# Performance work log

Measured on AMD Instinct MI355X. Metric: run time of the kernel, lower is better.

Reference implementation:

```python
import jax, jax.numpy as jnp
import numpy as np

WS = (8, 8, 8)          # window_size (d, h, w) -- all equal
N_TOK = WS[0] * WS[1] * WS[2]   # 512
DIM = 192
HEADS = 6
HEAD_DIM = DIM // HEADS  # 32
B_ = 64                  # num_windows * batch (batch = 1)


def _build_rel_coords_table():
    # matches torch: meshgrid of arange(-(w-1), w) per axis, normalized, *8, signed log2
    r = np.arange(-(WS[0] - 1), WS[0], dtype=np.float32)
    tab = np.stack(np.meshgrid(r, r, r, indexing='ij'), axis=-1)[None]  # (1,15,15,15,3)
    tab = tab / (WS[0] - 1)
    tab = tab * 8.0
    tab = np.sign(tab) * np.log2(np.abs(tab) + 1.0) / np.log2(8.0)
    return tab.astype(np.float32)


def _build_rel_pos_index():
    c = np.arange(WS[0])
    coords = np.stack(np.meshgrid(c, c, c, indexing='ij'))          # (3, 8, 8, 8)
    flat = coords.reshape(3, -1)                                     # (3, N)
    rel = flat[:, :, None] - flat[:, None, :]                        # (3, N, N)
    rel = rel.transpose(1, 2, 0).copy()                              # (N, N, 3)
    rel += WS[0] - 1
    rel[:, :, 0] *= (2 * WS[1] - 1) * (2 * WS[2] - 1)
    rel[:, :, 1] *= 2 * WS[2] - 1
    return rel.sum(-1).astype(np.int32)                              # (N, N)


def setup_inputs() -> dict:
    key = jax.random.key(0)
    ks = jax.random.split(key, 8)
    x = jax.random.normal(ks[0], (B_, N_TOK, DIM), dtype=jnp.float32)
    # 0 / -inf style additive mask (use large negative finite for stability)
    m = jax.random.uniform(ks[1], (B_, N_TOK, N_TOK))
    mask = jnp.where(m < 0.1, jnp.float32(-1e4), jnp.float32(0.0))
    w_qkv = jax.random.normal(ks[2], (3 * DIM, DIM), dtype=jnp.float32) * (DIM ** -0.5)
    q_bias = jnp.zeros((DIM,), jnp.float32)
    v_bias = jnp.zeros((DIM,), jnp.float32)
    cpb_w1 = jax.random.normal(ks[3], (512, 3), dtype=jnp.float32) * 0.3
    cpb_b1 = jnp.zeros((512,), jnp.float32)
    cpb_w2 = jax.random.normal(ks[4], (HEADS, 512), dtype=jnp.float32) * 0.05
    rel_coords_table = jnp.asarray(_build_rel_coords_table())
    rel_pos_index = jnp.asarray(_build_rel_pos_index())
    return {"x": x, "mask": mask, "w_qkv": w_qkv, "q_bias": q_bias,
            "v_bias": v_bias, "cpb_w1": cpb_w1, "cpb_b1": cpb_b1,
            "cpb_w2": cpb_w2, "rel_coords_table": rel_coords_table,
            "rel_pos_index": rel_pos_index}


def reference(x, mask, w_qkv, q_bias, v_bias, cpb_w1, cpb_b1, cpb_w2,
              rel_coords_table, rel_pos_index):
    Bw, N, C = x.shape
    H, D = HEADS, HEAD_DIM
    # qkv projection with bias = cat(q_bias, zeros, v_bias)
    qkv_bias = jnp.concatenate([q_bias, jnp.zeros_like(v_bias), v_bias])
    qkv = x @ w_qkv.T + qkv_bias                       # (Bw, N, 3C)
    qkv = qkv.reshape(Bw, N, 3, H, D).transpose(2, 0, 3, 1, 4)
    q, k, v = qkv[0], qkv[1], qkv[2]                   # (Bw, H, N, D)
    # continuous position bias MLP: 3 -> 512 -> H
    tab = rel_coords_table.reshape(-1, 3)              # (3375, 3)
    tab = jax.nn.relu(tab @ cpb_w1.T + cpb_b1) @ cpb_w2.T  # (3375, H)
    bias = tab[rel_pos_index.reshape(-1)].reshape(N, N, H)
    bias = 16.0 * jax.nn.sigmoid(bias.transpose(2, 0, 1))  # (H, N, N)
    # SDPA with additive mask (standard 1/sqrt(D) scaling, as in forward_flash)
    scale = jnp.float32(1.0 / np.sqrt(D))
    scores = jnp.einsum('bhnd,bhmd->bhnm', q, k) * scale
    scores = scores + mask[:, None, :, :] + bias[None]
    attn = jax.nn.softmax(scores, axis=-1)
    out = jnp.einsum('bhnm,bhmd->bhnd', attn, v)       # (Bw, H, N, D)
    return out
```

## Files before the change

kernel.cpp:

```cpp
#include <hip/hip_runtime.h>
#include <hip/hip_bf16.h>


typedef __bf16 bf16x8 __attribute__((ext_vector_type(8)));
typedef __bf16 bf16x4v __attribute__((ext_vector_type(4)));
typedef float  f32x4  __attribute__((ext_vector_type(4)));
typedef _Float16 f16x4 __attribute__((ext_vector_type(4)));
typedef _Float16 f16x8 __attribute__((ext_vector_type(8)));
typedef unsigned uint2v __attribute__((ext_vector_type(2)));
typedef int int4v __attribute__((ext_vector_type(4)));
typedef unsigned long long u64;

#define LOG2E 1.4426950408889634f

__device__ __forceinline__ bf16x8 cvt2_bf16x8(f32x4 a, f32x4 b) {
  bf16x8 r;
  r[0] = (__bf16)a[0]; r[1] = (__bf16)a[1]; r[2] = (__bf16)a[2]; r[3] = (__bf16)a[3];
  r[4] = (__bf16)b[0]; r[5] = (__bf16)b[1]; r[6] = (__bf16)b[2]; r[7] = (__bf16)b[3];
  return r;
}

__device__ __forceinline__ unsigned pack2bf(float a, float b) {
  unsigned short ua = __builtin_bit_cast(unsigned short, (__bf16)a);
  unsigned short ub = __builtin_bit_cast(unsigned short, (__bf16)b);
  return (unsigned)ua | ((unsigned)ub << 16);
}

__device__ __forceinline__ bf16x8 frag_from_words(unsigned w0, unsigned w1,
                                                  unsigned w2, unsigned w3) {
  union { unsigned u[4]; bf16x8 v; } f;
  f.u[0] = w0; f.u[1] = w1; f.u[2] = w2; f.u[3] = w3;
  return f.v;
}

#define PREP_MB    2048
#define PREP_WCONV 108
#define PREP_CPB   3375
#define PREP_GRID  (PREP_MB + PREP_WCONV + PREP_CPB)

__global__ __launch_bounds__(256) void prep_kernel(
    const float* __restrict__ w, __bf16* __restrict__ wbf,
    const float* __restrict__ table, const float* __restrict__ w1,
    const float* __restrict__ b1, const float* __restrict__ w2,
    float* __restrict__ tab6,
    const float* __restrict__ m, u64* __restrict__ bits)
{
  __shared__ float red[4][6];
  int blk = blockIdx.x;
  if (blk < PREP_MB) {
    int li8 = threadIdx.x & 7;
    for (size_t t = (size_t)blk * 256 + threadIdx.x;
         t < 2097152ull; t += (size_t)PREP_MB * 256) {
      const float* mp = m + t * 8;
      f32x4 v0 = *(const f32x4*)mp;
      f32x4 v1 = *(const f32x4*)(mp + 4);
      unsigned byte =
          (v0[0] == 0.f ? 1u : 0u)  | (v0[1] == 0.f ? 2u : 0u) |
          (v0[2] == 0.f ? 4u : 0u)  | (v0[3] == 0.f ? 8u : 0u) |
          (v1[0] == 0.f ? 16u : 0u) | (v1[1] == 0.f ? 32u : 0u) |
          (v1[2] == 0.f ? 64u : 0u) | (v1[3] == 0.f ? 128u : 0u);
      u64 part = (u64)byte << (8 * li8);
      part |= __shfl_xor(part, 1);
      part |= __shfl_xor(part, 2);
      part |= __shfl_xor(part, 4);
      if (li8 == 0) {
        int w_ = (int)(t >> 3);
        int b = w_ >> 12, i = (w_ >> 3) & 511, jw = w_ & 7;
        bits[(((size_t)b * 8 + jw) << 9) + i] = part;
      }
    }
  } else if (blk < PREP_MB + PREP_WCONV) {
    int t = (blk - PREP_MB) * 256 + threadIdx.x;
    f32x4 v = *(const f32x4*)(w + (size_t)t * 4);
    bf16x4v o;
    o[0] = (__bf16)v[0]; o[1] = (__bf16)v[1]; o[2] = (__bf16)v[2]; o[3] = (__bf16)v[3];
    *(bf16x4v*)(wbf + (size_t)t * 4) = o;
  } else {
    int p = blk - PREP_MB - PREP_WCONV;
    float c0 = table[p * 3 + 0], c1 = table[p * 3 + 1], c2 = table[p * 3 + 2];
    float acc[6] = {0.f, 0.f, 0.f, 0.f, 0.f, 0.f};
#pragma unroll
    for (int jj = 0; jj < 2; ++jj) {
      int j = threadIdx.x + jj * 256;
      float hv = w1[j * 3 + 0] * c0 + w1[j * 3 + 1] * c1 + w1[j * 3 + 2] * c2 + b1[j];
      hv = fmaxf(hv, 0.0f);
#pragma unroll
      for (int t = 0; t < 6; ++t) acc[t] += w2[t * 512 + j] * hv;
    }
#pragma unroll
    for (int t = 0; t < 6; ++t) {
      acc[t] += __shfl_xor(acc[t], 1);
      acc[t] += __shfl_xor(acc[t], 2);
      acc[t] += __shfl_xor(acc[t], 4);
      acc[t] += __shfl_xor(acc[t], 8);
      acc[t] += __shfl_xor(acc[t], 16);
      acc[t] += __shfl_xor(acc[t], 32);
    }
    int wave = threadIdx.x >> 6;
    if ((threadIdx.x & 63) == 0)
#pragma unroll
      for (int t = 0; t < 6; ++t) red[wave][t] = acc[t];
    __syncthreads();
    if (threadIdx.x < 6) {
      int t = threadIdx.x;
      float s = red[0][t] + red[1][t] + red[2][t] + red[3][t];
      float sig = 16.0f / (1.0f + expf(-s));
      tab6[p * 8 + t] = sig * LOG2E;
    }
  }
}

#define MID_QKV  3072
#define MID_BIAS 342
#define MID_GRID (MID_QKV + MID_BIAS)

__global__ __launch_bounds__(192) void mid_kernel(
    const float* __restrict__ x,
    const __bf16* __restrict__ wbf,
    const float* __restrict__ qb,
    const float* __restrict__ vb,
    __bf16* __restrict__ Qo,
    __bf16* __restrict__ Ko,
    __bf16* __restrict__ Vt,
    const int* __restrict__ relidx,
    const float* __restrict__ tab6,
    _Float16* __restrict__ biasH)
{
  __shared__ __bf16 tile[3][32][72];
  if (blockIdx.x >= MID_QKV) {
    for (int q4 = (blockIdx.x - MID_QKV) * 192 + threadIdx.x; q4 < 65536;
         q4 += MID_BIAS * 192) {
      int ij = q4 * 4;
      int i = ij >> 9, p = ij & 511;
      int jblk = p >> 6, g = (p >> 4) & 3, kf = (p >> 2) & 3;
      int j = (jblk << 6) + kf * 16 + g * 4;
      int4v idx4 = *(const int4v*)(relidx + (i << 9) + j);
      float val[6][4];
#pragma unroll
      for (int u = 0; u < 4; ++u) {
        f32x4 lo = *(const f32x4*)(tab6 + (size_t)idx4[u] * 8);
        f32x4 hi = *(const f32x4*)(tab6 + (size_t)idx4[u] * 8 + 4);
        val[0][u] = lo[0]; val[1][u] = lo[1]; val[2][u] = lo[2];
        val[3][u] = lo[3]; val[4][u] = hi[0]; val[5][u] = hi[1];
      }
#pragma unroll
      for (int t6 = 0; t6 < 6; ++t6) {
        f16x4 o = {(_Float16)val[t6][0], (_Float16)val[t6][1],
                   (_Float16)val[t6][2], (_Float16)val[t6][3]};
        *(f16x4*)(biasH + (size_t)t6 * 262144 + ij) = o;
      }
    }
    return;
  }
  const float CQ = 0.17677669529663687f * LOG2E;
  int region = blockIdx.x >> 10, rt = blockIdx.x & 1023;
  int lane = threadIdx.x & 63, wave = threadIdx.x >> 6;
  int g = lane >> 4, li = lane & 15;
  int rowbase = rt * 32;
  int b = rowbase >> 9, nbase = rowbase & 511;
  int nc = region * 3 + wave;

  bf16x8 a[2][6];
#pragma unroll
  for (int mm = 0; mm < 2; ++mm)
#pragma unroll
    for (int k = 0; k < 6; ++k) {
      const float* xp = x + (size_t)(rowbase + mm * 16 + li) * 192 + k * 32 + 8 * g;
      f32x4 x0 = *(const f32x4*)xp;
      f32x4 x1 = *(const f32x4*)(xp + 4);
      a[mm][k] = cvt2_bf16x8(x0, x1);
    }

  f32x4 acc[2][4];
#pragma unroll
  for (int n = 0; n < 4; ++n) {
    int r = nc * 64 + n * 16 + li;
    float bb = 0.0f;
    if (r < 192) bb = qb[r];
    else if (r >= 384) bb = vb[r - 384];
    f32x4 v = {bb, bb, bb, bb};
    acc[0][n] = v; acc[1][n] = v;
  }
#pragma unroll
  for (int k = 0; k < 6; ++k) {
#pragma unroll
    for (int n = 0; n < 4; ++n) {
      bf16x8 bf = *(const bf16x8*)(wbf + (size_t)(nc * 64 + n * 16 + li) * 192 + k * 32 + 8 * g);
      acc[0][n] = __builtin_amdgcn_mfma_f32_16x16x32_bf16(a[0][k], bf, acc[0][n], 0, 0, 0);
      acc[1][n] = __builtin_amdgcn_mfma_f32_16x16x32_bf16(a[1][k], bf, acc[1][n], 0, 0, 0);
    }
  }
  if (region < 2) {
    float scale = (region == 0) ? CQ : 1.0f;
#pragma unroll
    for (int n = 0; n < 4; ++n)
#pragma unroll
      for (int mm = 0; mm < 2; ++mm)
#pragma unroll
        for (int t = 0; t < 4; ++t)
          tile[wave][mm * 16 + 4 * g + t][n * 16 + li] = (__bf16)(acc[mm][n][t] * scale);
    int tok = lane & 31, hh = lane >> 5;
    int h = (nc * 2 + hh) % 6;
    __bf16* base = (region == 0) ? Qo : Ko;
    __bf16* dst = base + ((size_t)(b * 6 + h) * 512 + nbase + tok) * 32;
#pragma unroll
    for (int kq = 0; kq < 4; ++kq)
      *(bf16x8*)(dst + kq * 8) = *(const bf16x8*)&tile[wave][tok][hh * 32 + kq * 8];
  } else {
#pragma unroll
    for (int n = 0; n < 4; ++n) {
      int rr = nc * 64 + n * 16 + li - 384, h = rr >> 5, d = rr & 31;
#pragma unroll
      for (int mm = 0; mm < 2; ++mm) {
        int nn = nbase + mm * 16 + 4 * g;
        bf16x4v pk;
#pragma unroll
        for (int t = 0; t < 4; ++t) pk[t] = (__bf16)acc[mm][n][t];
        *(bf16x4v*)(Vt + ((size_t)(b * 6 + h) * 32 + d) * 512 + nn) = pk;
      }
    }
  }
}

__global__ __launch_bounds__(256, 3) void attn_kernel(
    const u64* __restrict__ bits,
    const _Float16* __restrict__ biasH,
    const __bf16* __restrict__ Qw,
    const __bf16* __restrict__ Kw,
    const __bf16* __restrict__ Vt,
    float* __restrict__ out)
{
  int hw = blockIdx.x;
  int xcd = hw & 7, seq = hw >> 3;
  int h = seq >> 4;
  int r = seq & 15;
  int b = xcd * 8 + (r >> 1);
  int qt = r & 1;
  int lane = threadIdx.x & 63, wave = threadIdx.x >> 6;
  int g = lane >> 4, li = lane & 15;
  int qbase = qt * 256 + wave * 64;
  int bh = b * 6 + h;
  int gsh = 4 * g;

  const __bf16* Qb = Qw + (size_t)bh * 16384;
  const __bf16* Kb = Kw + (size_t)bh * 16384;
  const __bf16* Vb = Vt + (size_t)bh * 16384;
  const _Float16* biasb = biasH + (size_t)h * 262144 + g * 16;
  const u64* bitsb = bits + (size_t)b * 4096;

  bf16x8 qfrag[4];
#pragma unroll
  for (int qf = 0; qf < 4; ++qf)
    qfrag[qf] = *(const bf16x8*)(Qb + (qbase + qf * 16 + li) * 32 + 8 * g);

  union { unsigned short us[8]; bf16x8 v; } onesu;
#pragma unroll
  for (int i = 0; i < 8; ++i) onesu.us[i] = 0x3F80;
  bf16x8 ones = onesu.v;

  f32x4 oacc[4][2] = {};
  f32x4 lacc[4] = {};

  for (int kb = 0; kb < 8; ++kb) {
    int j64 = kb * 64;
    unsigned mbl[4], mbh[4];
#pragma unroll
    for (int qf = 0; qf < 4; ++qf) {
      u64 m64 = bitsb[(kb << 9) + qbase + qf * 16 + li] >> gsh;
      mbl[qf] = (unsigned)m64;
      mbh[qf] = (unsigned)(m64 >> 32);
    }
    bf16x8 kfr[4];
#pragma unroll
    for (int kf = 0; kf < 4; ++kf)
      kfr[kf] = *(const bf16x8*)(Kb + (j64 + kf * 16 + li) * 32 + 8 * g);
    bf16x8 vfr[2][2];
#pragma unroll
    for (int df = 0; df < 2; ++df)
#pragma unroll
      for (int c = 0; c < 2; ++c)
        vfr[df][c] = *(const bf16x8*)(Vb + (df * 16 + li) * 512 + j64 + c * 32 + 8 * g);
    f16x8 hv8[4][2];
#pragma unroll
    for (int qf = 0; qf < 4; ++qf) {
      const _Float16* bp = biasb + (size_t)(qbase + qf * 16 + li) * 512 + j64;
      hv8[qf][0] = *(const f16x8*)(bp);
      hv8[qf][1] = *(const f16x8*)(bp + 8);
    }

    __builtin_amdgcn_s_setprio(1);
#pragma unroll
    for (int c = 0; c < 2; ++c) {
      unsigned lo[4][2], hi[4][2];
#pragma unroll
      for (int kfl = 0; kfl < 2; ++kfl) {
        int kf = c * 2 + kfl;
        const int hsel = kf >> 1, hoff = (kf & 1) * 4;
        const int bb0 = (kf & 1) * 16;
#pragma unroll
        for (int qf = 0; qf < 4; ++qf) {
          f16x8 hb = hv8[qf][hsel];
          f32x4 ci = {(float)hb[hoff], (float)hb[hoff + 1],
                      (float)hb[hoff + 2], (float)hb[hoff + 3]};
          f32x4 s = __builtin_amdgcn_mfma_f32_16x16x32_bf16(kfr[kf], qfrag[qf], ci, 0, 0, 0);
          unsigned mword = hsel ? mbh[qf] : mbl[qf];
          unsigned m0 = (unsigned)((int)(mword << (31 - (bb0 + 0))) >> 31);
          unsigned m1 = (unsigned)((int)(mword << (31 - (bb0 + 1))) >> 31);
          unsigned m2 = (unsigned)((int)(mword << (31 - (bb0 + 2))) >> 31);
          unsigned m3 = (unsigned)((int)(mword << (31 - (bb0 + 3))) >> 31);
          float p0 = __builtin_bit_cast(float,
              __builtin_bit_cast(unsigned, __builtin_amdgcn_exp2f(s[0])) & m0);
          float p1 = __builtin_bit_cast(float,
              __builtin_bit_cast(unsigned, __builtin_amdgcn_exp2f(s[1])) & m1);
          float p2 = __builtin_bit_cast(float,
              __builtin_bit_cast(unsigned, __builtin_amdgcn_exp2f(s[2])) & m2);
          float p3 = __builtin_bit_cast(float,
              __builtin_bit_cast(unsigned, __builtin_amdgcn_exp2f(s[3])) & m3);
          lo[qf][kfl] = pack2bf(p0, p1);
          hi[qf][kfl] = pack2bf(p2, p3);
        }
      }
#pragma unroll
      for (int qf = 0; qf < 4; ++qf) {
        uint2v sl = __builtin_amdgcn_permlane32_swap(lo[qf][0], lo[qf][1], 0, 0);
        uint2v wl = __builtin_amdgcn_permlane16_swap(sl.x, sl.y, 0, 0);
        uint2v sh = __builtin_amdgcn_permlane32_swap(hi[qf][0], hi[qf][1], 0, 0);
        uint2v wh = __builtin_amdgcn_permlane16_swap(sh.x, sh.y, 0, 0);
        bf16x8 pf = frag_from_words(wl.x, wh.x, wl.y, wh.y);
        oacc[qf][0] = __builtin_amdgcn_mfma_f32_16x16x32_bf16(vfr[0][c], pf, oacc[qf][0], 0, 0, 0);
        oacc[qf][1] = __builtin_amdgcn_mfma_f32_16x16x32_bf16(vfr[1][c], pf, oacc[qf][1], 0, 0, 0);
        lacc[qf]    = __builtin_amdgcn_mfma_f32_16x16x32_bf16(ones, pf, lacc[qf], 0, 0, 0);
      }
    }
    __builtin_amdgcn_s_setprio(0);
  }

#pragma unroll
  for (int qf = 0; qf < 4; ++qf) {
    float linv = 1.0f / lacc[qf][0];
#pragma unroll
    for (int df = 0; df < 2; ++df) {
      float* op = out + ((size_t)bh * 512 + qbase + qf * 16 + li) * 32 + df * 16 + 4 * g;
      f32x4 r2 = oacc[qf][df] * linv;
      *(f32x4*)op = r2;
    }
  }
}

extern "C" void kernel_launch(void* const* d_in, const int* in_sizes, int n_in,
                              void* d_out, int out_size, void* d_ws, size_t ws_size,
                              hipStream_t stream) {
  const float* x    = (const float*)d_in[0];
  const float* mask = (const float*)d_in[1];
  const float* wqkv = (const float*)d_in[2];
  const float* qb   = (const float*)d_in[3];
  const float* vb   = (const float*)d_in[4];
  const float* w1   = (const float*)d_in[5];
  const float* b1   = (const float*)d_in[6];
  const float* w2   = (const float*)d_in[7];
  const float* tbl  = (const float*)d_in[8];
  const int*   ridx = (const int*)d_in[9];
  float* out = (float*)d_out;

  char* ws = (char*)d_ws;
  float*    tab6  = (float*)(ws);
  _Float16* biasH = (_Float16*)(ws + 131072);
  u64*      bits  = (u64*)(ws + 131072 + 3145728);
  __bf16*   wbf   = (__bf16*)(ws + 131072 + 3145728 + 2097152);
  __bf16*   Q     = (__bf16*)(ws + 131072 + 3145728 + 2097152 + 262144);
  __bf16*   K     = Q + (size_t)64 * 6 * 512 * 32;
  __bf16*   Vt    = K + (size_t)64 * 6 * 512 * 32;

  prep_kernel<<<PREP_GRID, 256, 0, stream>>>(wqkv, wbf, tbl, w1, b1, w2, tab6,
                                             mask, bits);
  mid_kernel<<<MID_GRID, 192, 0, stream>>>(x, wbf, qb, vb, Q, K, Vt,
                                           ridx, tab6, biasH);
  attn_kernel<<<768, 256, 0, stream>>>(bits, biasH, Q, K, Vt, out);
}
```

Before: 126.1 us.

## Fuse QKV projection into attention kernel with Q/K/V staged in shared memory

The QKV projection is moved into the attention kernel. Each 512-thread block computes Q, K and V for one (window, head) pair directly into LDS, so Q/K/Vt no longer make a round trip through global memory. The bias gather is split out into its own small kernel. In exchange, x is read once per head and the LDS footprint is large, and the block now covers all 512 queries with 384 blocks instead of 768, which reduces parallelism and occupancy.

Measured after the change: 122.2 us. -3.1%, faster.

```diff
diff --git a/kernel.cpp b/kernel.cpp
--- a/kernel.cpp
+++ b/kernel.cpp
@@ -110,148 +110,129 @@
   }
 }
 
-#define MID_QKV  3072
-#define MID_BIAS 342
-#define MID_GRID (MID_QKV + MID_BIAS)
-
-__global__ __launch_bounds__(192) void mid_kernel(
+__global__ __launch_bounds__(256) void bias_kernel(
+    const int* __restrict__ relidx,
+    const float* __restrict__ tab6,
+    _Float16* __restrict__ biasH)
+{
+  int q4 = blockIdx.x * 256 + threadIdx.x;
+  int ij = q4 * 4;
+  int i = ij >> 9, p = ij & 511;
+  int jblk = p >> 6, g = (p >> 4) & 3, kf = (p >> 2) & 3;
+  int j = (jblk << 6) + kf * 16 + g * 4;
+  int4v idx4 = *(const int4v*)(relidx + (i << 9) + j);
+  float val[6][4];
+#pragma unroll
+  for (int u = 0; u < 4; ++u) {
+    f32x4 lo = *(const f32x4*)(tab6 + (size_t)idx4[u] * 8);
+    f32x4 hi = *(const f32x4*)(tab6 + (size_t)idx4[u] * 8 + 4);
+    val[0][u] = lo[0]; val[1][u] = lo[1]; val[2][u] = lo[2];
+    val[3][u] = lo[3]; val[4][u] = hi[0]; val[5][u] = hi[1];
+  }
+#pragma unroll
+  for (int t6 = 0; t6 < 6; ++t6) {
+    f16x4 o = {(_Float16)val[t6][0], (_Float16)val[t6][1],
+               (_Float16)val[t6][2], (_Float16)val[t6][3]};
+    *(f16x4*)(biasH + (size_t)t6 * 262144 + ij) = o;
+  }
+}
+
+#define FUSED_GRID 384
+
+__global__ __launch_bounds__(512, 2) void fused_kernel(
     const float* __restrict__ x,
     const __bf16* __restrict__ wbf,
     const float* __restrict__ qb,
     const float* __restrict__ vb,
-    __bf16* __restrict__ Qo,
-    __bf16* __restrict__ Ko,
-    __bf16* __restrict__ Vt,
-    const int* __restrict__ relidx,
-    const float* __restrict__ tab6,
-    _Float16* __restrict__ biasH)
+    const u64* __restrict__ bits,
+    const _Float16* __restrict__ biasH,
+    float* __restrict__ out)
 {
-  __shared__ __bf16 tile[3][32][72];
-  if (blockIdx.x >= MID_QKV) {
-    for (int q4 = (blockIdx.x - MID_QKV) * 192 + threadIdx.x; q4 < 65536;
-         q4 += MID_BIAS * 192) {
-      int ij = q4 * 4;
-      int i = ij >> 9, p = ij & 511;
-      int jblk = p >> 6, g = (p >> 4) & 3, kf = (p >> 2) & 3;
-      int j = (jblk << 6) + kf * 16 + g * 4;
-      int4v idx4 = *(const int4v*)(relidx + (i << 9) + j);
-      float val[6][4];
-#pragma unroll
-      for (int u = 0; u < 4; ++u) {
-        f32x4 lo = *(const f32x4*)(tab6 + (size_t)idx4[u] * 8);
-        f32x4 hi = *(const f32x4*)(tab6 + (size_t)idx4[u] * 8 + 4);
-        val[0][u] = lo[0]; val[1][u] = lo[1]; val[2][u] = lo[2];
-        val[3][u] = lo[3]; val[4][u] = hi[0]; val[5][u] = hi[1];
-      }
-#pragma unroll
-      for (int t6 = 0; t6 < 6; ++t6) {
-        f16x4 o = {(_Float16)val[t6][0], (_Float16)val[t6][1],
-                   (_Float16)val[t6][2], (_Float16)val[t6][3]};
-        *(f16x4*)(biasH + (size_t)t6 * 262144 + ij) = o;
-      }
-    }
-    return;
-  }
-  const float CQ = 0.17677669529663687f * LOG2E;
-  int region = blockIdx.x >> 10, rt = blockIdx.x & 1023;
+  __shared__ __bf16 Qs[512][40];
+  __shared__ __bf16 Ks[512][40];
+  __shared__ __bf16 Vs[32][520];
+
+  int blk = blockIdx.x;
+  int xcd = blk & 7, seq = blk >> 3;
+  int h = seq >> 3;
+  int b = xcd * 8 + (seq & 7);
   int lane = threadIdx.x & 63, wave = threadIdx.x >> 6;
   int g = lane >> 4, li = lane & 15;
-  int rowbase = rt * 32;
-  int b = rowbase >> 9, nbase = rowbase & 511;
-  int nc = region * 3 + wave;
-
-  bf16x8 a[2][6];
-#pragma unroll
-  for (int mm = 0; mm < 2; ++mm)
-#pragma unroll
-    for (int k = 0; k < 6; ++k) {
-      const float* xp = x + (size_t)(rowbase + mm * 16 + li) * 192 + k * 32 + 8 * g;
-      f32x4 x0 = *(const f32x4*)xp;
-      f32x4 x1 = *(const f32x4*)(xp + 4);
-      a[mm][k] = cvt2_bf16x8(x0, x1);
-    }
-
-  f32x4 acc[2][4];
-#pragma unroll
-  for (int n = 0; n < 4; ++n) {
-    int r = nc * 64 + n * 16 + li;
-    float bb = 0.0f;
-    if (r < 192) bb = qb[r];
-    else if (r >= 384) bb = vb[r - 384];
-    f32x4 v = {bb, bb, bb, bb};
-    acc[0][n] = v; acc[1][n] = v;
-  }
-#pragma unroll
-  for (int k = 0; k < 6; ++k) {
-#pragma unroll
-    for (int n = 0; n < 4; ++n) {
-      bf16x8 bf = *(const bf16x8*)(wbf + (size_t)(nc * 64 + n * 16 + li) * 192 + k * 32 + 8 * g);
-      acc[0][n] = __builtin_amdgcn_mfma_f32_16x16x32_bf16(a[0][k], bf, acc[0][n], 0, 0, 0);
-      acc[1][n] = __builtin_amdgcn_mfma_f32_16x16x32_bf16(a[1][k], bf, acc[1][n], 0, 0, 0);
-    }
-  }
-  if (region < 2) {
-    float scale = (region == 0) ? CQ : 1.0f;
-#pragma unroll
-    for (int n = 0; n < 4; ++n)
-#pragma unroll
-      for (int mm = 0; mm < 2; ++mm)
-#pragma unroll
-        for (int t = 0; t < 4; ++t)
-          tile[wave][mm * 16 + 4 * g + t][n * 16 + li] = (__bf16)(acc[mm][n][t] * scale);
-    int tok = lane & 31, hh = lane >> 5;
-    int h = (nc * 2 + hh) % 6;
-    __bf16* base = (region == 0) ? Qo : Ko;
-    __bf16* dst = base + ((size_t)(b * 6 + h) * 512 + nbase + tok) * 32;
-#pragma unroll
-    for (int kq = 0; kq < 4; ++kq)
-      *(bf16x8*)(dst + kq * 8) = *(const bf16x8*)&tile[wave][tok][hh * 32 + kq * 8];
-  } else {
-#pragma unroll
-    for (int n = 0; n < 4; ++n) {
-      int rr = nc * 64 + n * 16 + li - 384, h = rr >> 5, d = rr & 31;
-#pragma unroll
-      for (int mm = 0; mm < 2; ++mm) {
-        int nn = nbase + mm * 16 + 4 * g;
-        bf16x4v pk;
-#pragma unroll
-        for (int t = 0; t < 4; ++t) pk[t] = (__bf16)acc[mm][n][t];
-        *(bf16x4v*)(Vt + ((size_t)(b * 6 + h) * 32 + d) * 512 + nn) = pk;
-      }
-    }
-  }
-}
-
-__global__ __launch_bounds__(256, 3) void attn_kernel(
-    const u64* __restrict__ bits,
-    const _Float16* __restrict__ biasH,
-    const __bf16* __restrict__ Qw,
-    const __bf16* __restrict__ Kw,
-    const __bf16* __restrict__ Vt,
-    float* __restrict__ out)
-{
-  int hw = blockIdx.x;
-  int xcd = hw & 7, seq = hw >> 3;
-  int h = seq >> 4;
-  int r = seq & 15;
-  int b = xcd * 8 + (r >> 1);
-  int qt = r & 1;
-  int lane = threadIdx.x & 63, wave = threadIdx.x >> 6;
-  int g = lane >> 4, li = lane & 15;
-  int qbase = qt * 256 + wave * 64;
   int bh = b * 6 + h;
   int gsh = 4 * g;
-
-  const __bf16* Qb = Qw + (size_t)bh * 16384;
-  const __bf16* Kb = Kw + (size_t)bh * 16384;
-  const __bf16* Vb = Vt + (size_t)bh * 16384;
+  const float CQ = 0.17677669529663687f * LOG2E;
+
+  {
+    const __bf16* wp[6];
+    float bb[6];
+#pragma unroll
+    for (int n = 0; n < 6; ++n) {
+      int wcol, reg = n >> 1, sub = n & 1;
+      int d = sub * 16 + li;
+      wcol = reg * 192 + h * 32 + d;
+      wp[n] = wbf + (size_t)wcol * 192 + 8 * g;
+      bb[n] = (reg == 0) ? qb[wcol] : (reg == 2 ? vb[h * 32 + d] : 0.0f);
+    }
+#pragma unroll
+    for (int mi = 0; mi < 2; ++mi) {
+      int rowb = wave * 64 + mi * 32;
+      bf16x8 a[2][6];
+#pragma unroll
+      for (int mm = 0; mm < 2; ++mm)
+#pragma unroll
+        for (int k = 0; k < 6; ++k) {
+          const float* xp = x + (size_t)(b * 512 + rowb + mm * 16 + li) * 192 + k * 32 + 8 * g;
+          f32x4 x0 = *(const f32x4*)xp;
+          f32x4 x1 = *(const f32x4*)(xp + 4);
+          a[mm][k] = cvt2_bf16x8(x0, x1);
+        }
+      f32x4 acc[2][6];
+#pragma unroll
+      for (int n = 0; n < 6; ++n) {
+        f32x4 v = {bb[n], bb[n], bb[n], bb[n]};
+        acc[0][n] = v; acc[1][n] = v;
+      }
+#pragma unroll
+      for (int k = 0; k < 6; ++k)
+#pragma unroll
+        for (int n = 0; n < 6; ++n) {
+          bf16x8 bf = *(const bf16x8*)(wp[n] + k * 32);
+          acc[0][n] = __builtin_amdgcn_mfma_f32_16x16x32_bf16(a[0][k], bf, acc[0][n], 0, 0, 0);
+          acc[1][n] = __builtin_amdgcn_mfma_f32_16x16x32_bf16(a[1][k], bf, acc[1][n], 0, 0, 0);
+        }
+#pragma unroll
+      for (int mm = 0; mm < 2; ++mm) {
+        int tok0 = rowb + mm * 16 + 4 * g;
+#pragma unroll
+        for (int n = 0; n < 2; ++n)
+#pragma unroll
+          for (int t = 0; t < 4; ++t)
+            Qs[tok0 + t][n * 16 + li] = (__bf16)(acc[mm][n][t] * CQ);
+#pragma unroll
+        for (int n = 2; n < 4; ++n)
+#pragma unroll
+          for (int t = 0; t < 4; ++t)
+            Ks[tok0 + t][(n - 2) * 16 + li] = (__bf16)acc[mm][n][t];
+#pragma unroll
+        for (int n = 4; n < 6; ++n) {
+          bf16x4v pk;
+#pragma unroll
+          for (int t = 0; t < 4; ++t) pk[t] = (__bf16)acc[mm][n][t];
+          *(bf16x4v*)&Vs[(n - 4) * 16 + li][tok0] = pk;
+        }
+      }
+    }
+  }
+  __syncthreads();
+
+  int qbase = wave * 64;
   const _Float16* biasb = biasH + (size_t)h * 262144 + g * 16;
   const u64* bitsb = bits + (size_t)b * 4096;
 
   bf16x8 qfrag[4];
 #pragma unroll
   for (int qf = 0; qf < 4; ++qf)
-    qfrag[qf] = *(const bf16x8*)(Qb + (qbase + qf * 16 + li) * 32 + 8 * g);
+    qfrag[qf] = *(const bf16x8*)&Qs[qbase + qf * 16 + li][8 * g];
 
   union { unsigned short us[8]; bf16x8 v; } onesu;
 #pragma unroll
@@ -273,17 +254,17 @@
     bf16x8 kfr[4];
 #pragma unroll
     for (int kf = 0; kf < 4; ++kf)
-      kfr[kf] = *(const bf16x8*)(Kb + (j64 + kf * 16 + li) * 32 + 8 * g);
+      kfr[kf] = *(const bf16x8*)&Ks[j64 + kf * 16 + li][8 * g];
     bf16x8 vfr[2][2];
 #pragma unroll
     for (int df = 0; df < 2; ++df)
 #pragma unroll
       for (int c = 0; c < 2; ++c)
-        vfr[df][c] = *(const bf16x8*)(Vb + (df * 16 + li) * 512 + j64 + c * 32 + 8 * g);
+        vfr[df][c] = *(const bf16x8*)&Vs[df * 16 + li][j64 + c * 32 + 8 * g];
     f16x8 hv8[4][2];
 #pragma unroll
     for (int qf = 0; qf < 4; ++qf) {
-      const _Float16* bp = biasb + (size_t)(qbase + qf * 16 + li) * 512 + j64;
+      const _Float16* bp = biasb + (qbase + qf * 16 + li) * 512 + j64;
       hv8[qf][0] = *(const f16x8*)(bp);
       hv8[qf][1] = *(const f16x8*)(bp + 8);
     }
@@ -367,13 +348,9 @@
   _Float16* biasH = (_Float16*)(ws + 131072);
   u64*      bits  = (u64*)(ws + 131072 + 3145728);
   __bf16*   wbf   = (__bf16*)(ws + 131072 + 3145728 + 2097152);
-  __bf16*   Q     = (__bf16*)(ws + 131072 + 3145728 + 2097152 + 262144);
-  __bf16*   K     = Q + (size_t)64 * 6 * 512 * 32;
-  __bf16*   Vt    = K + (size_t)64 * 6 * 512 * 32;
 
   prep_kernel<<<PREP_GRID, 256, 0, stream>>>(wqkv, wbf, tbl, w1, b1, w2, tab6,
                                              mask, bits);
-  mid_kernel<<<MID_GRID, 192, 0, stream>>>(x, wbf, qb, vb, Q, K, Vt,
-                                           ridx, tab6, biasH);
-  attn_kernel<<<768, 256, 0, stream>>>(bits, biasH, Q, K, Vt, out);
-}
+  bias_kernel<<<256, 256, 0, stream>>>(ridx, tab6, biasH);
+  fused_kernel<<<FUSED_GRID, 512, 0, stream>>>(x, wbf, qb, vb, bits, biasH, out);
+}
```
